# Performance work log

Measured on AMD Instinct MI355X. Metric: run time of the kernel, lower is better.

## Reference

```python
import jax, jax.numpy as jnp
import numpy as np

B = 16; H = 64; WRES = 64; C = 512; NH = 16; WH = 8; WW = 8; PATCH = 4
N = WH * WW; HD = C // NH; R_MAX = PATCH * H; HID = 4 * C
PI = 3.141592653589793


def _rel_coords():
    yy, xx = np.meshgrid(np.arange(WH), np.arange(WW), indexing='ij')
    flat = np.stack([yy.ravel(), xx.ravel()])  # (2, N)
    rel = flat[:, :, None] - flat[:, None, :]  # (2, N, N)
    return rel[0].astype(np.int32), rel[1].astype(np.int32)

RAD_NP, AZ_NP = _rel_coords()


def _ln(x, g, b):
    m = x.mean(-1, keepdims=True)
    v = ((x - m) ** 2).mean(-1, keepdims=True)
    return (x - m) / jnp.sqrt(v + 1e-5) * g + b


def setup_inputs() -> dict:
    key = jax.random.key(0)
    ks = jax.random.split(key, 12)
    s = 0.02
    return {
        'x': jax.random.normal(ks[0], (B, H * WRES, C), jnp.float32),
        'D': jax.random.uniform(ks[1], (B, H, WRES), jnp.float32),
        'norm1_g': jnp.ones((C,), jnp.float32), 'norm1_b': jnp.zeros((C,), jnp.float32),
        'qkv_w': jax.random.normal(ks[2], (3 * C, C), jnp.float32) * s,
        'qkv_b': jnp.zeros((3 * C,), jnp.float32),
        'proj_w': jax.random.normal(ks[3], (C, C), jnp.float32) * s,
        'proj_b': jnp.zeros((C,), jnp.float32),
        'a_p': jax.random.normal(ks[4], (2 * WW - 1, NH), jnp.float32) * s,
        'b_p': jax.random.normal(ks[5], (2 * WW - 1, NH), jnp.float32) * s,
        'a_r': jax.random.normal(ks[6], (2 * WH - 1, NH), jnp.float32) * s,
        'b_r': jax.random.normal(ks[7], (2 * WH - 1, NH), jnp.float32) * s,
        'norm2_g': jnp.ones((C,), jnp.float32), 'norm2_b': jnp.zeros((C,), jnp.float32),
        'fc1_w': jax.random.normal(ks[8], (HID, C), jnp.float32) * s,
        'fc1_b': jnp.zeros((HID,), jnp.float32),
        'fc2_w': jax.random.normal(ks[9], (C, HID), jnp.float32) * s,
        'fc2_b': jnp.zeros((C,), jnp.float32),
    }


def reference(x, D, norm1_g, norm1_b, qkv_w, qkv_b, proj_w, proj_b,
              a_p, b_p, a_r, b_r, norm2_g, norm2_b, fc1_w, fc1_b, fc2_w, fc2_b):
    rad = jnp.asarray(RAD_NP)  # (N, N) relative row offsets in [-(WH-1), WH-1]
    az = jnp.asarray(AZ_NP)    # (N, N) relative col offsets
    shortcut = x
    xn = _ln(x, norm1_g, norm1_b).reshape(B, H, WRES, C)
    # window partition: (B,H,W,C) -> (nW*B, N, C); same for D -> (nW*B, N)
    xw = xn.reshape(B, H // WH, WH, WRES // WW, WW, C).transpose(0, 1, 3, 2, 4, 5).reshape(-1, N, C)
    Dw = D.reshape(B, H // WH, WH, WRES // WW, WW).transpose(0, 1, 3, 2, 4).reshape(-1, N)
    # qkv: (B_, N, 3C) -> q,k,v (B_, NH, N, HD)
    qkv = (xw @ qkv_w.T + qkv_b).reshape(-1, N, 3, NH, HD).transpose(2, 0, 3, 1, 4)
    q, k, v = qkv[0], qkv[1], qkv[2]
    q = q * (HD ** -0.5)
    attn = jnp.einsum('bhnd,bhmd->bhnm', q, k)
    # A_phi: gathered azimuth tables + trig, (N, N, NH). torch negative index == idx % size
    ip = az % (2 * WW - 1)
    azf = az.astype(jnp.float32) * (2.0 * PI / WRES)
    A_phi = a_p[ip] * jnp.cos(azf)[..., None] + b_p[ip] * jnp.sin(azf)[..., None]
    # A_r: per-window depth-modulated radius, (B_, N, N, NH); rad_final[b,i,j] = rad[i,j]*D[b,j]
    ir = rad % (2 * WH - 1)
    ang = (rad.astype(jnp.float32)[None] * Dw[:, None, :]) * (2.0 * PI / R_MAX)
    A_r = a_r[ir][None] * jnp.cos(ang)[..., None] + b_r[ir][None] * jnp.sin(ang)[..., None]
    attn = attn + jnp.transpose(A_phi, (2, 0, 1))[None] + jnp.transpose(A_r, (0, 3, 1, 2))
    attn = jax.nn.softmax(attn, axis=-1)
    out = jnp.einsum('bhnm,bhmd->bhnd', attn, v).transpose(0, 2, 1, 3).reshape(-1, N, C)
    out = out @ proj_w.T + proj_b
    # window reverse -> (B, H*W, C)
    xr = out.reshape(B, H // WH, WRES // WW, WH, WW, C).transpose(0, 1, 3, 2, 4, 5).reshape(B, H * WRES, C)
    x = shortcut + xr
    xm = _ln(x, norm2_g, norm2_b)
    h = jax.nn.gelu(xm @ fc1_w.T + fc1_b, approximate=False)
    return x + (h @ fc2_w.T + fc2_b)
```

## Files before the change

kernel.cpp:

```cpp
#include <hip/hip_runtime.h>
#include <hip/hip_bf16.h>
#include <math.h>

typedef __hip_bfloat16 bf16;
using f32x4  = __attribute__((ext_vector_type(4))) float;
using bf16x8 = __attribute__((ext_vector_type(8))) short;

static __device__ __forceinline__ float b2f(bf16 v) { return __bfloat162float(v); }
static __device__ __forceinline__ short f2b_s(float f) {
    bf16 b = __float2bfloat16(f);
    return *reinterpret_cast<short*>(&b);
}

static __device__ __forceinline__ void gl_lds16(const void* g, void* l) {
    __builtin_amdgcn_global_load_lds(
        (const __attribute__((address_space(1))) unsigned int*)g,
        (__attribute__((address_space(3))) unsigned int*)l, 16, 0, 0);
}

__global__ __launch_bounds__(256) void f2b_kernel(const float* __restrict__ in,
                                                  short* __restrict__ out, int n4)
{
    int i = blockIdx.x * 256 + threadIdx.x;
    if (i < n4) {
        float4 f = reinterpret_cast<const float4*>(in)[i];
        short4 s;
        s.x = f2b_s(f.x); s.y = f2b_s(f.y); s.z = f2b_s(f.z); s.w = f2b_s(f.w);
        reinterpret_cast<short4*>(out)[i] = s;
    }
}

__global__ __launch_bounds__(64) void ln_kernel(
    const float* __restrict__ in, const float* __restrict__ g,
    const float* __restrict__ bta, bf16* __restrict__ out, int windowed)
{
    int lr  = blockIdx.x;
    int tid = threadIdx.x;
    const float* xr = in + (size_t)lr * 512;
    int c0 = tid * 8;
    float4 f0 = *reinterpret_cast<const float4*>(xr + c0);
    float4 f1 = *reinterpret_cast<const float4*>(xr + c0 + 4);
    float v[8] = { f0.x, f0.y, f0.z, f0.w, f1.x, f1.y, f1.z, f1.w };
    float s = 0.f, s2 = 0.f;
#pragma unroll
    for (int k = 0; k < 8; ++k) { s += v[k]; s2 += v[k] * v[k]; }
#pragma unroll
    for (int off = 32; off; off >>= 1) {
        s  += __shfl_xor(s,  off, 64);
        s2 += __shfl_xor(s2, off, 64);
    }
    float mean = s * (1.0f / 512.0f);
    float var  = s2 * (1.0f / 512.0f) - mean * mean;
    float inv  = rsqrtf(var + 1e-5f);
    size_t drow;
    if (windowed) {
        int b_loc = lr >> 12;
        int l  = lr & 4095;
        int gr = l >> 6, gc = l & 63;
        int wy = gr >> 3, iy = gr & 7, wx = gc >> 3, ix = gc & 7;
        drow = (size_t)((b_loc * 64 + wy * 8 + wx) * 64 + iy * 8 + ix);
    } else {
        drow = (size_t)lr;
    }
    bf16* orow = out + drow * 512;
#pragma unroll
    for (int k = 0; k < 8; ++k) {
        int c = c0 + k;
        orow[c] = __float2bfloat16((v[k] - mean) * inv * g[c] + bta[c]);
    }
}

__global__ __launch_bounds__(256) void gemm_mfma(
    const bf16* __restrict__ A, const short* __restrict__ W,
    const float* __restrict__ bias, int N, int K, int mode,
    void* __restrict__ dstv, const float* __restrict__ res)
{
    __shared__ short Asl[128 * 32];
    __shared__ short Bsl[128 * 32];

    int tid  = threadIdx.x;
    int wave = tid >> 6, lane = tid & 63;
    int waveM = wave >> 1, waveN = wave & 1;
    int mBase = blockIdx.y * 128;
    int nBase = blockIdx.x * 128;

    f32x4 acc[4][4] = {};

    int rr   = wave * 32 + (lane >> 2);
    int segE = (lane & 3) * 8;
    const bf16*  Ag = A + (size_t)(mBase + rr) * K + segE;
    const short* Bg = W + (size_t)(nBase + rr) * K + segE;
    short* Al0 = &Asl[wave * 1024];
    short* Bl0 = &Bsl[wave * 1024];

    int mf = waveM * 64 + (lane & 15);
    int nf = waveN * 64 + (lane & 15);
    int kq = (lane >> 4) * 8;

    for (int kb = 0; kb < K; kb += 32) {
        gl_lds16(Ag + kb,               Al0);
        gl_lds16(Ag + kb + (size_t)16 * K, Al0 + 512);
        gl_lds16(Bg + kb,               Bl0);
        gl_lds16(Bg + kb + (size_t)16 * K, Bl0 + 512);
        __syncthreads();

        bf16x8 af[4], bfv[4];
#pragma unroll
        for (int i = 0; i < 4; ++i)
            af[i] = *reinterpret_cast<const bf16x8*>(&Asl[(mf + i * 16) * 32 + kq]);
#pragma unroll
        for (int j = 0; j < 4; ++j)
            bfv[j] = *reinterpret_cast<const bf16x8*>(&Bsl[(nf + j * 16) * 32 + kq]);
#pragma unroll
        for (int i = 0; i < 4; ++i)
#pragma unroll
            for (int j = 0; j < 4; ++j)
                acc[i][j] = __builtin_amdgcn_mfma_f32_16x16x32_bf16(af[i], bfv[j], acc[i][j], 0, 0, 0);
        __syncthreads();
    }

    int rq = (lane >> 4) * 4;
#pragma unroll
    for (int j = 0; j < 4; ++j) {
        int n = nBase + waveN * 64 + j * 16 + (lane & 15);
        float bn = bias[n];
#pragma unroll
        for (int i = 0; i < 4; ++i) {
#pragma unroll
            for (int reg = 0; reg < 4; ++reg) {
                int m = mBase + waveM * 64 + i * 16 + rq + reg;
                float v = acc[i][j][reg] + bn;
                if (mode == 0) {
                    ((bf16*)dstv)[(size_t)m * N + n] = __float2bfloat16(v);
                } else if (mode == 1) {
                    int b_loc = m >> 12, w = (m >> 6) & 63, tk = m & 63;
                    int wy = w >> 3, wx = w & 7, iy = tk >> 3, ix = tk & 7;
                    int l = ((wy << 3) + iy) * 64 + (wx << 3) + ix;
                    size_t idx = ((size_t)(b_loc * 4096 + l)) * 512 + n;
                    ((float*)dstv)[idx] = v + res[idx];
                } else if (mode == 2) {
                    float gl = 0.5f * v * (1.0f + erff(v * 0.70710678118654752f));
                    ((bf16*)dstv)[(size_t)m * N + n] = __float2bfloat16(gl);
                } else {
                    size_t idx = (size_t)m * N + n;
                    ((float*)dstv)[idx] = v + res[idx];
                }
            }
        }
    }
}

__global__ __launch_bounds__(64) void attn_kernel(
    const bf16* __restrict__ qkv, const float* __restrict__ Dofs,
    const float* __restrict__ a_p, const float* __restrict__ b_p,
    const float* __restrict__ a_r, const float* __restrict__ b_r,
    bf16* __restrict__ xattn)
{
    __shared__ float Ksh[64][32];
    __shared__ float Vsh[64][32];
    __shared__ float Ssh[64][65];
    __shared__ float Dsh[64];
    __shared__ float aps[15], bps[15], ars[15], brs[15];

    int bid = blockIdx.x;
    int h   = bid & 15;
    int b_  = bid >> 4;
    int bl  = b_ >> 6;
    int w   = b_ & 63;
    int wy = w >> 3, wx = w & 7;
    int i = threadIdx.x;

    const bf16* kp = qkv + (size_t)(b_ * 64 + i) * 1536 + 512 + h * 32;
    const bf16* vp = kp + 512;
#pragma unroll
    for (int d = 0; d < 32; ++d) {
        Ksh[i][d] = b2f(kp[d]);
        Vsh[i][d] = b2f(vp[d]);
    }
    {
        int jy = i >> 3, jx = i & 7;
        Dsh[i] = Dofs[(size_t)bl * 4096 + (wy * 8 + jy) * 64 + (wx * 8 + jx)];
    }
    if (i < 15) {
        aps[i] = a_p[i * 16 + h]; bps[i] = b_p[i * 16 + h];
        ars[i] = a_r[i * 16 + h]; brs[i] = b_r[i * 16 + h];
    }
    __syncthreads();

    float q[32];
    const bf16* qp = qkv + (size_t)(b_ * 64 + i) * 1536 + h * 32;
#pragma unroll
    for (int d = 0; d < 32; ++d) q[d] = b2f(qp[d]);

    const float scale = 0.17677669529663687f;
    const float c_az  = 0.09817477042468103f;
    const float c_r   = 0.02454369260617026f;
    int iy = i >> 3, ix = i & 7;

    float mx = -1e30f;
    for (int j = 0; j < 64; ++j) {
        float dot = 0.f;
#pragma unroll
        for (int d = 0; d < 32; ++d) dot += q[d] * Ksh[j][d];
        int jy = j >> 3, jx = j & 7;
        int az = ix - jx, rad = iy - jy;
        int ip = az  < 0 ? az  + 15 : az;
        int ir = rad < 0 ? rad + 15 : rad;
        float azf  = az * c_az;
        float aphi = aps[ip] * __cosf(azf) + bps[ip] * __sinf(azf);
        float ang  = rad * Dsh[j] * c_r;
        float arv  = ars[ir] * __cosf(ang) + brs[ir] * __sinf(ang);
        float sc = dot * scale + aphi + arv;
        Ssh[i][j] = sc;
        mx = fmaxf(mx, sc);
    }
    float sum = 0.f;
    for (int j = 0; j < 64; ++j) {
        float e = __expf(Ssh[i][j] - mx);
        Ssh[i][j] = e;
        sum += e;
    }
    float inv = 1.0f / sum;
    float acc[32] = {};
    for (int j = 0; j < 64; ++j) {
        float p = Ssh[i][j];
#pragma unroll
        for (int d = 0; d < 32; ++d) acc[d] += p * Vsh[j][d];
    }
    bf16* op = xattn + (size_t)(b_ * 64 + i) * 512 + h * 32;
#pragma unroll
    for (int d = 0; d < 32; ++d) op[d] = __float2bfloat16(acc[d] * inv);
}

extern "C" void kernel_launch(void* const* d_in, const int* in_sizes, int n_in,
                              void* d_out, int out_size, void* d_ws, size_t ws_size,
                              hipStream_t stream)
{
    const float* x      = (const float*)d_in[0];
    const float* D      = (const float*)d_in[1];
    const float* n1g    = (const float*)d_in[2];
    const float* n1b    = (const float*)d_in[3];
    const float* qkv_w  = (const float*)d_in[4];
    const float* qkv_b  = (const float*)d_in[5];
    const float* proj_w = (const float*)d_in[6];
    const float* proj_b = (const float*)d_in[7];
    const float* a_p    = (const float*)d_in[8];
    const float* b_p    = (const float*)d_in[9];
    const float* a_r    = (const float*)d_in[10];
    const float* b_r    = (const float*)d_in[11];
    const float* n2g    = (const float*)d_in[12];
    const float* n2b    = (const float*)d_in[13];
    const float* fc1_w  = (const float*)d_in[14];
    const float* fc1_b  = (const float*)d_in[15];
    const float* fc2_w  = (const float*)d_in[16];
    const float* fc2_b  = (const float*)d_in[17];
    float* out = (float*)d_out;

    char* ws = (char*)d_ws;
    short* qkv_wb  = (short*)ws;
    short* proj_wb = qkv_wb + 786432;
    short* fc1_wb  = proj_wb + 262144;
    short* fc2_wb  = fc1_wb + 1048576;
    char* gws = (char*)(fc2_wb + 1048576);

    int G = 16;
    while (G > 1 && 6291456 + (size_t)G * 4096 * 7168 > ws_size) G >>= 1;
    int NG = 16 / G;
    size_t rowsA = (size_t)G * 4096;

    float* x2   = (float*)gws;
    bf16*  xw   = (bf16*)(gws + rowsA * 2048);
    bf16*  qkvb = xw + rowsA * 512;
    bf16*  xatt = qkvb + rowsA * 1536;
    bf16*  xm   = xw;
    bf16*  hbuf = qkvb;

    hipLaunchKernelGGL(f2b_kernel, dim3(768),  dim3(256), 0, stream, qkv_w,  qkv_wb,  196608);
    hipLaunchKernelGGL(f2b_kernel, dim3(256),  dim3(256), 0, stream, proj_w, proj_wb,  65536);
    hipLaunchKernelGGL(f2b_kernel, dim3(1024), dim3(256), 0, stream, fc1_w,  fc1_wb,  262144);
    hipLaunchKernelGGL(f2b_kernel, dim3(1024), dim3(256), 0, stream, fc2_w,  fc2_wb,  262144);

    int gy = (int)(rowsA / 128);

    for (int g = 0; g < NG; ++g) {
        size_t r0 = (size_t)g * rowsA;
        hipLaunchKernelGGL(ln_kernel, dim3((int)rowsA), dim3(64), 0, stream,
                           x + r0 * 512, n1g, n1b, xw, 1);
        hipLaunchKernelGGL(gemm_mfma, dim3(1536 / 128, gy), dim3(256), 0, stream,
                           xw, qkv_wb, qkv_b, 1536, 512, 0, (void*)qkvb, (const float*)nullptr);
        hipLaunchKernelGGL(attn_kernel, dim3(G * 1024), dim3(64), 0, stream,
                           qkvb, D + r0, a_p, b_p, a_r, b_r, xatt);
        hipLaunchKernelGGL(gemm_mfma, dim3(512 / 128, gy), dim3(256), 0, stream,
                           xatt, proj_wb, proj_b, 512, 512, 1, (void*)x2, x + r0 * 512);
        hipLaunchKernelGGL(ln_kernel, dim3((int)rowsA), dim3(64), 0, stream,
                           x2, n2g, n2b, xm, 0);
        hipLaunchKernelGGL(gemm_mfma, dim3(2048 / 128, gy), dim3(256), 0, stream,
                           xm, fc1_wb, fc1_b, 2048, 512, 2, (void*)hbuf, (const float*)nullptr);
        hipLaunchKernelGGL(gemm_mfma, dim3(512 / 128, gy), dim3(256), 0, stream,
                           hbuf, fc2_wb, fc2_b, 512, 2048, 3, (void*)(out + r0 * 512), x2);
    }
}
```

Before: 1.699 ms.

## Rewrite window attention with MFMA, one block per window across all heads

Replaces the scalar per-head, per-thread attention kernel with a 256-thread block per window that loops over the 16 heads. QK^T and PV now run on bf16 MFMA instructions, and softmax uses cross-lane shuffles. The cos/sin tables for the depth-modulated radius and the azimuth bias are precomputed once per window in LDS and reused by every head, so far fewer transcendental calls are needed. In exchange, the probabilities are rounded to bf16 before the PV product and the block count drops sixteenfold.

```diff
diff --git a/kernel.cpp b/kernel.cpp
--- a/kernel.cpp
+++ b/kernel.cpp
@@ -150,86 +150,142 @@
     }
 }
 
-__global__ __launch_bounds__(64) void attn_kernel(
+__global__ __launch_bounds__(256) void attn_kernel(
     const bf16* __restrict__ qkv, const float* __restrict__ Dofs,
     const float* __restrict__ a_p, const float* __restrict__ b_p,
     const float* __restrict__ a_r, const float* __restrict__ b_r,
     bf16* __restrict__ xattn)
 {
-    __shared__ float Ksh[64][32];
-    __shared__ float Vsh[64][32];
-    __shared__ float Ssh[64][65];
-    __shared__ float Dsh[64];
-    __shared__ float aps[15], bps[15], ars[15], brs[15];
-
-    int bid = blockIdx.x;
-    int h   = bid & 15;
-    int b_  = bid >> 4;
-    int bl  = b_ >> 6;
-    int w   = b_ & 63;
+    __shared__ float cosr[15][64];
+    __shared__ float sinr[15][64];
+    __shared__ float aphiS[15][16];
+    __shared__ float arsS[15][16];
+    __shared__ float brsS[15][16];
+    __shared__ short Vt[32][72];
+    __shared__ short Psh[64][72];
+
+    int b_ = blockIdx.x;
+    int bl = b_ >> 6;
+    int w  = b_ & 63;
     int wy = w >> 3, wx = w & 7;
-    int i = threadIdx.x;
-
-    const bf16* kp = qkv + (size_t)(b_ * 64 + i) * 1536 + 512 + h * 32;
-    const bf16* vp = kp + 512;
-#pragma unroll
-    for (int d = 0; d < 32; ++d) {
-        Ksh[i][d] = b2f(kp[d]);
-        Vsh[i][d] = b2f(vp[d]);
-    }
-    {
-        int jy = i >> 3, jx = i & 7;
-        Dsh[i] = Dofs[(size_t)bl * 4096 + (wy * 8 + jy) * 64 + (wx * 8 + jx)];
-    }
-    if (i < 15) {
-        aps[i] = a_p[i * 16 + h]; bps[i] = b_p[i * 16 + h];
-        ars[i] = a_r[i * 16 + h]; brs[i] = b_r[i * 16 + h];
-    }
-    __syncthreads();
-
-    float q[32];
-    const bf16* qp = qkv + (size_t)(b_ * 64 + i) * 1536 + h * 32;
-#pragma unroll
-    for (int d = 0; d < 32; ++d) q[d] = b2f(qp[d]);
+    int tid  = threadIdx.x;
+    int wave = tid >> 6, lane = tid & 63;
 
     const float scale = 0.17677669529663687f;
     const float c_az  = 0.09817477042468103f;
     const float c_r   = 0.02454369260617026f;
-    int iy = i >> 3, ix = i & 7;
-
-    float mx = -1e30f;
-    for (int j = 0; j < 64; ++j) {
-        float dot = 0.f;
-#pragma unroll
-        for (int d = 0; d < 32; ++d) dot += q[d] * Ksh[j][d];
+
+    for (int t = tid; t < 960; t += 256) {
+        int k = t >> 6;
+        int j = t & 63;
         int jy = j >> 3, jx = j & 7;
-        int az = ix - jx, rad = iy - jy;
-        int ip = az  < 0 ? az  + 15 : az;
-        int ir = rad < 0 ? rad + 15 : rad;
-        float azf  = az * c_az;
-        float aphi = aps[ip] * __cosf(azf) + bps[ip] * __sinf(azf);
-        float ang  = rad * Dsh[j] * c_r;
-        float arv  = ars[ir] * __cosf(ang) + brs[ir] * __sinf(ang);
-        float sc = dot * scale + aphi + arv;
-        Ssh[i][j] = sc;
-        mx = fmaxf(mx, sc);
-    }
-    float sum = 0.f;
-    for (int j = 0; j < 64; ++j) {
-        float e = __expf(Ssh[i][j] - mx);
-        Ssh[i][j] = e;
-        sum += e;
-    }
-    float inv = 1.0f / sum;
-    float acc[32] = {};
-    for (int j = 0; j < 64; ++j) {
-        float p = Ssh[i][j];
-#pragma unroll
-        for (int d = 0; d < 32; ++d) acc[d] += p * Vsh[j][d];
-    }
-    bf16* op = xattn + (size_t)(b_ * 64 + i) * 512 + h * 32;
-#pragma unroll
-    for (int d = 0; d < 32; ++d) op[d] = __float2bfloat16(acc[d] * inv);
+        float Dj  = Dofs[(size_t)bl * 4096 + (wy * 8 + jy) * 64 + (wx * 8 + jx)];
+        float ang = (float)(k - 7) * Dj * c_r;
+        cosr[k][j] = __cosf(ang);
+        sinr[k][j] = __sinf(ang);
+    }
+    if (tid < 240) {
+        int k = tid >> 4;
+        int h = tid & 15;
+        int v = k - 7;
+        int ip = v < 0 ? v + 15 : v;
+        float azf = (float)v * c_az;
+        aphiS[k][h] = a_p[ip * 16 + h] * __cosf(azf) + b_p[ip * 16 + h] * __sinf(azf);
+        arsS[k][h]  = a_r[ip * 16 + h];
+        brsS[k][h]  = b_r[ip * 16 + h];
+    }
+
+    int i_blk = wave;
+    int l15 = lane & 15;
+    int lq  = lane >> 4;
+    int m0  = i_blk * 16 + lq * 4;
+    const bf16* qbase = qkv + (size_t)(b_ * 64) * 1536;
+    bf16* obase = xattn + (size_t)(b_ * 64) * 512;
+
+    for (int h = 0; h < 16; ++h) {
+        __syncthreads();
+        {
+            int tok = tid >> 2, dc = (tid & 3) * 8;
+            bf16x8 vv = *reinterpret_cast<const bf16x8*>(
+                qkv + (size_t)(b_ * 64 + tok) * 1536 + 1024 + h * 32 + dc);
+#pragma unroll
+            for (int s = 0; s < 8; ++s) Vt[dc + s][tok] = vv[s];
+        }
+        __syncthreads();
+
+        bf16x8 af = *reinterpret_cast<const bf16x8*>(
+            qbase + (size_t)(i_blk * 16 + l15) * 1536 + h * 32 + lq * 8);
+        f32x4 Sacc[4] = {};
+#pragma unroll
+        for (int jb = 0; jb < 4; ++jb) {
+            bf16x8 kf = *reinterpret_cast<const bf16x8*>(
+                qbase + (size_t)(jb * 16 + l15) * 1536 + 512 + h * 32 + lq * 8);
+            Sacc[jb] = __builtin_amdgcn_mfma_f32_16x16x32_bf16(af, kf, Sacc[jb], 0, 0, 0);
+        }
+
+        float Sv[4][4];
+        float inv[4];
+#pragma unroll
+        for (int reg = 0; reg < 4; ++reg) {
+            int m = m0 + reg;
+            int iy = m >> 3, ix = m & 7;
+            float rmax = -1e30f;
+#pragma unroll
+            for (int jb = 0; jb < 4; ++jb) {
+                int n = jb * 16 + l15;
+                int jy = n >> 3, jx = n & 7;
+                int ai = ix - jx + 7;
+                int ri = iy - jy + 7;
+                float sc = Sacc[jb][reg] * scale + aphiS[ai][h]
+                         + arsS[ri][h] * cosr[ri][n] + brsS[ri][h] * sinr[ri][n];
+                Sv[reg][jb] = sc;
+                rmax = fmaxf(rmax, sc);
+            }
+#pragma unroll
+            for (int off = 1; off <= 8; off <<= 1)
+                rmax = fmaxf(rmax, __shfl_xor(rmax, off, 64));
+            float rsum = 0.f;
+#pragma unroll
+            for (int jb = 0; jb < 4; ++jb) {
+                float e = __expf(Sv[reg][jb] - rmax);
+                Sv[reg][jb] = e;
+                rsum += e;
+            }
+#pragma unroll
+            for (int off = 1; off <= 8; off <<= 1)
+                rsum += __shfl_xor(rsum, off, 64);
+            inv[reg] = 1.0f / rsum;
+        }
+
+#pragma unroll
+        for (int reg = 0; reg < 4; ++reg)
+#pragma unroll
+            for (int jb = 0; jb < 4; ++jb)
+                Psh[m0 + reg][jb * 16 + l15] = f2b_s(Sv[reg][jb]);
+
+        f32x4 o[2] = {};
+#pragma unroll
+        for (int ks = 0; ks < 2; ++ks) {
+            bf16x8 pa = *reinterpret_cast<const bf16x8*>(
+                &Psh[i_blk * 16 + l15][ks * 32 + lq * 8]);
+#pragma unroll
+            for (int nb = 0; nb < 2; ++nb) {
+                bf16x8 bv = *reinterpret_cast<const bf16x8*>(
+                    &Vt[nb * 16 + l15][ks * 32 + lq * 8]);
+                o[nb] = __builtin_amdgcn_mfma_f32_16x16x32_bf16(pa, bv, o[nb], 0, 0, 0);
+            }
+        }
+
+#pragma unroll
+        for (int nb = 0; nb < 2; ++nb) {
+            int d = nb * 16 + l15;
+#pragma unroll
+            for (int reg = 0; reg < 4; ++reg) {
+                int m = m0 + reg;
+                obase[(size_t)m * 512 + h * 32 + d] = __float2bfloat16(o[nb][reg] * inv[reg]);
+            }
+        }
+    }
 }
 
 extern "C" void kernel_launch(void* const* d_in, const int* in_sizes, int n_in,
@@ -288,7 +344,7 @@
                            x + r0 * 512, n1g, n1b, xw, 1);
         hipLaunchKernelGGL(gemm_mfma, dim3(1536 / 128, gy), dim3(256), 0, stream,
                            xw, qkv_wb, qkv_b, 1536, 512, 0, (void*)qkvb, (const float*)nullptr);
-        hipLaunchKernelGGL(attn_kernel, dim3(G * 1024), dim3(64), 0, stream,
+        hipLaunchKernelGGL(attn_kernel, dim3(G * 64), dim3(256), 0, stream,
                            qkvb, D + r0, a_p, b_p, a_r, b_r, xatt);
         hipLaunchKernelGGL(gemm_mfma, dim3(512 / 128, gy), dim3(256), 0, stream,
                            xatt, proj_wb, proj_b, 512, 512, 1, (void*)x2, x + r0 * 512);
```

Result: faster. 1.417 ms (-16.6%).
